# Kernel tuning notes

Hardware: AMD Instinct MI355X
Metric: run time of the kernel (lower is better)

## Reference

```python
import jax, jax.numpy as jnp
import numpy as np

L_RTN = 3  # complex taps produced by the RTN head (w_rtn3 out dim = 2*L_RTN)
EPS = 1e-12


def _to_complex(x):
    # (B, 2n) real interleaved [re0, im0, re1, im1, ...] -> (B, n) complex
    return x[:, 0::2] + 1j * x[:, 1::2]


def _to_real(xc):
    # (B, n) complex -> (B, 2n) real interleaved
    b, n = xc.shape
    return jnp.stack([xc.real, xc.imag], axis=-1).reshape(b, 2 * n)


def _complex_conv_taps(h_c, x_c):
    # per-sample causal complex FIR: out[t] = sum_l h[l] * x[t-l]
    # h_c: (B, L) complex, x_c: (B, n) complex
    n = x_c.shape[1]
    out = jnp.zeros_like(x_c)
    for l in range(h_c.shape[1]):  # L is tiny and static
        shifted = jnp.pad(x_c, ((0, 0), (l, 0)))[:, :n]
        out = out + h_c[:, l:l + 1] * shifted
    return out


def setup_inputs() -> dict:
    key = jax.random.key(0)
    ks = jax.random.split(key, 16)
    B, D_IN, H1, CH, H_RTN, H2, D_OUT = 8192, 512, 4096, 256, 1024, 4096, 512
    s = 0.02  # weight init scale
    x = jax.random.normal(ks[0], (B, D_IN), jnp.float32)
    w1 = s * jax.random.normal(ks[1], (H1, D_IN), jnp.float32)
    b1 = jnp.zeros((H1,), jnp.float32)
    w2 = s * jax.random.normal(ks[2], (CH, H1), jnp.float32)
    b2 = jnp.zeros((CH,), jnp.float32)
    w_rtn1 = s * jax.random.normal(ks[3], (H_RTN, CH), jnp.float32)
    b_rtn1 = jnp.zeros((H_RTN,), jnp.float32)
    w_rtn2 = s * jax.random.normal(ks[4], (H_RTN, H_RTN), jnp.float32)
    b_rtn2 = jnp.zeros((H_RTN,), jnp.float32)
    w_rtn3 = s * jax.random.normal(ks[5], (2 * L_RTN, H_RTN), jnp.float32)
    # bias so that RTN starts near identity tap [1, 0, 0, ...]
    b_rtn3 = jnp.zeros((2 * L_RTN,), jnp.float32).at[0].set(1.0)
    w3 = s * jax.random.normal(ks[6], (H2, CH), jnp.float32)
    b3 = jnp.zeros((H2,), jnp.float32)
    w4 = s * jax.random.normal(ks[7], (D_OUT, H2), jnp.float32)
    b4 = jnp.zeros((D_OUT,), jnp.float32)
    h = jax.random.normal(ks[8], (2,), jnp.float32)
    h = h / jnp.linalg.norm(h)  # unit-power single-tap fading channel
    noise = 0.1 * jax.random.normal(ks[9], (B, CH), jnp.float32)
    return {"x": x, "w1": w1, "b1": b1, "w2": w2, "b2": b2,
            "w_rtn1": w_rtn1, "b_rtn1": b_rtn1, "w_rtn2": w_rtn2,
            "b_rtn2": b_rtn2, "w_rtn3": w_rtn3, "b_rtn3": b_rtn3,
            "w3": w3, "b3": b3, "w4": w4, "b4": b4, "h": h, "noise": noise}


def reference(x, w1, b1, w2, b2, w_rtn1, b_rtn1, w_rtn2, b_rtn2,
              w_rtn3, b_rtn3, w3, b3, w4, b4, h, noise):
    # encoder (linear1 -> relu -> linear2)
    a = jax.nn.relu(x @ w1.T + b1)
    s = a @ w2.T + b2                      # (B, 2n) channel signal
    # power normalization: sqrt(2n) * sqrt(0.5) * s / ||s||
    scale = jnp.sqrt(s.shape[1] * 0.5)
    s = scale * s / jnp.linalg.norm(s, axis=1, keepdims=True)
    tx_c = _to_complex(s)                  # (B, n) transmitted symbols
    # single-tap complex channel
    h_c = h[0] + 1j * h[1]
    y = _to_real(h_c * tx_c) + noise       # add per-sample AWGN
    y_c = _to_complex(y)
    # LS channel estimate (1 tap): h_est = <y, x> / <x, x>
    num = jnp.sum(y_c * jnp.conj(tx_c), axis=1, keepdims=True)
    den = jnp.sum(jnp.abs(tx_c) ** 2, axis=1, keepdims=True)
    h_est = num / den                      # (B, 1)
    # zero-forcing signal estimate
    x_eq = y_c * jnp.conj(h_est) / (jnp.abs(h_est) ** 2 + EPS)
    xr = _to_real(x_eq)                    # (B, 2n)
    # RTN: predict inverse taps and apply per-sample complex conv
    g = jnp.tanh(xr @ w_rtn1.T + b_rtn1)
    g = jnp.tanh(g @ w_rtn2.T + b_rtn2)
    h_inv = g @ w_rtn3.T + b_rtn3          # (B, 2*L_RTN)
    h_inv_c = h_inv[:, 0::2] + 1j * h_inv[:, 1::2]
    xr = _to_real(_complex_conv_taps(h_inv_c, _to_complex(xr)))
    # decoder (linear3 -> relu -> linear4)
    out = jax.nn.relu(xr @ w3.T + b3)
    return out @ w4.T + b4
```

## Files before the change

### kernel.cpp

```cpp
#include <hip/hip_runtime.h>
#include <hip/hip_bf16.h>
#include <math.h>

using bf16 = __hip_bfloat16;
typedef __attribute__((ext_vector_type(8))) short short8;
typedef __attribute__((ext_vector_type(4))) float float4v;

template <typename T> __device__ inline T cvt_out(float v);
template <> __device__ inline float cvt_out<float>(float v) { return v; }
template <> __device__ inline bf16 cvt_out<bf16>(float v) { return __float2bfloat16(v); }

__device__ inline void gload_lds16(const bf16* g, bf16* l) {
    __builtin_amdgcn_global_load_lds(
        (const __attribute__((address_space(1))) void*)g,
        (__attribute__((address_space(3))) void*)l, 16, 0, 0);
}

struct CvtPack {
    const float* src[7];
    bf16* dst[7];
    int end[7];
};

__global__ __launch_bounds__(256) void cvt_all(CvtPack p) {
    int e = (blockIdx.x * 256 + threadIdx.x) * 4;
    int start = 0;
#pragma unroll
    for (int s = 0; s < 7; ++s) {
        if (e < p.end[s]) {
            int off = e - start;
            float4 v = *(const float4*)(p.src[s] + off);
            bf16* d = p.dst[s] + off;
            d[0] = __float2bfloat16(v.x);
            d[1] = __float2bfloat16(v.y);
            d[2] = __float2bfloat16(v.z);
            d[3] = __float2bfloat16(v.w);
            return;
        }
        start = p.end[s];
    }
}

__device__ inline float4 load4f(const float* p) { return *(const float4*)p; }
__device__ inline float4 load4f(const bf16* p) {
    ushort4 u = *(const ushort4*)p;
    float4 r;
    r.x = __uint_as_float((unsigned)u.x << 16);
    r.y = __uint_as_float((unsigned)u.y << 16);
    r.z = __uint_as_float((unsigned)u.z << 16);
    r.w = __uint_as_float((unsigned)u.w << 16);
    return r;
}
__device__ inline void store4(float* p, float4 v) { *(float4*)p = v; }
__device__ inline void store4(bf16* p, float4 v) {
    p[0] = __float2bfloat16(v.x); p[1] = __float2bfloat16(v.y);
    p[2] = __float2bfloat16(v.z); p[3] = __float2bfloat16(v.w);
}

template <int NK, int ACT, typename InT, typename OutT>
__global__ __launch_bounds__(256) void reduceK(const InT* __restrict__ p,
                                               const float* __restrict__ bias,
                                               OutT* __restrict__ out,
                                               size_t mn, int nmask, int total4) {
    int i = blockIdx.x * 256 + threadIdx.x;
    if (i < total4) {
        int idx = i * 4;
        float4 r = *(const float4*)(bias + (idx & nmask));
#pragma unroll
        for (int k = 0; k < NK; ++k) {
            float4 a = load4f(p + k * mn + idx);
            r.x += a.x; r.y += a.y; r.z += a.z; r.w += a.w;
        }
        if (ACT == 1) {
            r.x = fmaxf(r.x, 0.f); r.y = fmaxf(r.y, 0.f);
            r.z = fmaxf(r.z, 0.f); r.w = fmaxf(r.w, 0.f);
        } else if (ACT == 2) {
            r.x = tanhf(r.x); r.y = tanhf(r.y);
            r.z = tanhf(r.z); r.w = tanhf(r.w);
        }
        store4(out + idx, r);
    }
}

template <int ACT, typename OutT, bool PARTIAL>
__global__ __launch_bounds__(512, 2)
void gemm_pipe8(const bf16* __restrict__ A,
                const bf16* __restrict__ W,
                const float* __restrict__ bias,
                OutT* __restrict__ C,
                int M, int N, int K,
                int nbn, int kcount) {
    constexpr int BKT = 64;
    constexpr int CPR = BKT / 8;
    constexpr int LPH = BKT / 32;
    constexpr int KS  = BKT / 32;

    __shared__ bf16 As[2][2][128 * BKT];
    __shared__ bf16 Bs[2][2][128 * BKT];

    const int bi = blockIdx.x;
    const int xcd = bi & 7, t = bi >> 3;
    const int bn = t % nbn;
    const int bm = xcd + 8 * (t / nbn);
    const int kbeg = PARTIAL ? blockIdx.y * kcount : 0;
    OutT* Cp = PARTIAL ? C + (size_t)blockIdx.y * M * N : C;

    const int tid = threadIdx.x;
    const int wave = tid >> 6, lane = tid & 63;
    const int mwave = (wave >> 2) * 64, nwave = (wave & 3) * 32;
    const int quad = lane >> 4, lrow = lane & 15;
    const int swz = lrow & (CPR - 1);

    const bf16* Ab = A + (size_t)(bm * 256) * K + kbeg;
    const bf16* Wb = W + (size_t)(bn * 256) * K + kbeg;
    const int NT = kcount / BKT;

    auto stA = [&](int tl, int h) {
        if (tl >= NT) return;
#pragma unroll
        for (int tt = 0; tt < LPH; ++tt) {
            int base = tt * 512 + wave * 64;
            int c = base + lane;
            int row = c / CPR, ch = c % CPR;
            gload_lds16(Ab + (size_t)(h * 128 + row) * K + tl * BKT +
                            ((ch ^ (row & (CPR - 1))) << 3),
                        &As[tl & 1][h][0] + base * 8);
        }
    };
    auto stB = [&](int tl, int h) {
        if (tl >= NT) return;
#pragma unroll
        for (int tt = 0; tt < LPH; ++tt) {
            int base = tt * 512 + wave * 64;
            int c = base + lane;
            int row = c / CPR, ch = c % CPR;
            gload_lds16(Wb + (size_t)(h * 128 + row) * K + tl * BKT +
                            ((ch ^ (row & (CPR - 1))) << 3),
                        &Bs[tl & 1][h][0] + base * 8);
        }
    };

    float4v acc[2][2][4][2] = {};
    short8 af[4][KS], bfv[2][KS];

#define LDA8(BUF, MH)                                                         \
    { const bf16* pA = &As[BUF][MH][0];                                       \
      _Pragma("unroll") for (int i = 0; i < 4; ++i)                           \
        _Pragma("unroll") for (int ks = 0; ks < KS; ++ks)                     \
          af[i][ks] = *(const short8*)(pA + (mwave + i * 16 + lrow) * BKT +   \
                                       (((ks * 4 + quad) ^ swz) << 3)); }
#define LDB8(BUF, NH)                                                         \
    { const bf16* pB = &Bs[BUF][NH][0];                                       \
      _Pragma("unroll") for (int j = 0; j < 2; ++j)                           \
        _Pragma("unroll") for (int ks = 0; ks < KS; ++ks)                     \
          bfv[j][ks] = *(const short8*)(pB + (nwave + j * 16 + lrow) * BKT +  \
                                        (((ks * 4 + quad) ^ swz) << 3)); }
#define MM8(MH, NH)                                                           \
    { _Pragma("unroll") for (int ks = 0; ks < KS; ++ks)                       \
        _Pragma("unroll") for (int i = 0; i < 4; ++i)                         \
          _Pragma("unroll") for (int j = 0; j < 2; ++j)                       \
            acc[MH][NH][i][j] = __builtin_amdgcn_mfma_f32_16x16x32_bf16(      \
                af[i][ks], bfv[j][ks], acc[MH][NH][i][j], 0, 0, 0); }
#define WAITC asm volatile("s_waitcnt vmcnt(4)" ::: "memory");
#define SYNC_IN                                                               \
    __builtin_amdgcn_s_barrier();                                             \
    __builtin_amdgcn_s_setprio(1);
#define SYNC_OUT                                                              \
    __builtin_amdgcn_s_setprio(0);                                            \
    __builtin_amdgcn_s_barrier();

    stA(0, 0); stB(0, 0); stA(0, 1); stB(0, 1);
    stA(1, 0); stB(1, 1);
    if (NT > 1) { WAITC; }
    else        asm volatile("s_waitcnt vmcnt(0)" ::: "memory");
    __builtin_amdgcn_s_barrier();

    for (int T = 0; T < NT; T += 2) {
        LDA8(0, 0); LDB8(0, 0); stA(T + 1, 1);
        SYNC_IN; MM8(0, 0); SYNC_OUT;
        LDB8(0, 1); stB(T + 1, 0);
        SYNC_IN; MM8(0, 1); SYNC_OUT;
        LDA8(0, 1); stA(T + 2, 0);
        SYNC_IN; MM8(1, 1); SYNC_OUT;
        LDB8(0, 0); stB(T + 2, 1);
        SYNC_IN; MM8(1, 0);
        __builtin_amdgcn_s_setprio(0);
        if (T + 2 < NT) { WAITC; }
        else            asm volatile("s_waitcnt vmcnt(0)" ::: "memory");
        __builtin_amdgcn_s_barrier();
        LDA8(1, 0); LDB8(1, 0); stA(T + 2, 1);
        SYNC_IN; MM8(0, 0); SYNC_OUT;
        LDB8(1, 1); stB(T + 2, 0);
        SYNC_IN; MM8(0, 1); SYNC_OUT;
        LDA8(1, 1); stA(T + 3, 0);
        SYNC_IN; MM8(1, 1); SYNC_OUT;
        LDB8(1, 0); stB(T + 3, 1);
        SYNC_IN; MM8(1, 0);
        __builtin_amdgcn_s_setprio(0);
        if (T + 2 < NT) {
            WAITC;
            __builtin_amdgcn_s_barrier();
        }
    }
#undef LDA8
#undef LDB8
#undef MM8
#undef WAITC
#undef SYNC_IN
#undef SYNC_OUT

#pragma unroll
    for (int mh = 0; mh < 2; ++mh)
#pragma unroll
        for (int i = 0; i < 4; ++i) {
            int m0 = bm * 256 + mh * 128 + mwave + i * 16 + quad * 4;
#pragma unroll
            for (int nh = 0; nh < 2; ++nh)
#pragma unroll
                for (int j = 0; j < 2; ++j) {
                    int n = bn * 256 + nh * 128 + nwave + j * 16 + lrow;
                    if constexpr (PARTIAL) {
#pragma unroll
                        for (int r = 0; r < 4; ++r)
                            Cp[(size_t)(m0 + r) * N + n] = cvt_out<OutT>(acc[mh][nh][i][j][r]);
                    } else {
                        float bv = bias[n];
#pragma unroll
                        for (int r = 0; r < 4; ++r) {
                            float v = acc[mh][nh][i][j][r] + bv;
                            if (ACT == 1) v = fmaxf(v, 0.f);
                            else if (ACT == 2) v = tanhf(v);
                            Cp[(size_t)(m0 + r) * N + n] = cvt_out<OutT>(v);
                        }
                    }
                }
        }
}

template <int ACT, typename OutT, int WMT, int WNT, int BKT, bool PARTIAL>
__global__ __launch_bounds__(256) void gemm_bt(const bf16* __restrict__ A,
                                               const bf16* __restrict__ W,
                                               const float* __restrict__ bias,
                                               OutT* __restrict__ C,
                                               int M, int N, int K,
                                               int nbn, int kcount) {
    constexpr int TBM = 32 * WMT;
    constexpr int TBN = 32 * WNT;
    constexpr int CPR = BKT / 8;
    constexpr int CA = TBM * CPR;
    constexpr int CB = TBN * CPR;

    __shared__ bf16 As[TBM * BKT];
    __shared__ bf16 Bs[TBN * BKT];

    const int bi = blockIdx.x;
    const int xcd = bi & 7, t = bi >> 3;
    const int bn = t % nbn;
    const int bm = xcd + 8 * (t / nbn);
    const int kbeg = PARTIAL ? blockIdx.y * kcount : 0;
    OutT* Cp = PARTIAL ? C + (size_t)blockIdx.y * M * N : C;

    const int tid = threadIdx.x;
    const int wave = tid >> 6, lane = tid & 63;
    const int wm = (wave >> 1) * (16 * WMT), wn = (wave & 1) * (16 * WNT);
    const int quad = lane >> 4, lrow = lane & 15;

    float4v acc[WMT][WNT] = {};
    const size_t arow = (size_t)(bm * TBM) * K;
    const size_t brow = (size_t)(bn * TBN) * K;

    for (int k0 = kbeg; k0 < kbeg + kcount; k0 += BKT) {
        __syncthreads();
#pragma unroll
        for (int tt = 0; tt < CA / 256; ++tt) {
            int base = tt * 256 + wave * 64;
            int c = base + lane;
            int row = c / CPR, col = (c % CPR) * 8;
            gload_lds16(A + arow + (size_t)row * K + k0 + col, As + base * 8);
        }
#pragma unroll
        for (int tt = 0; tt < CB / 256; ++tt) {
            int base = tt * 256 + wave * 64;
            int c = base + lane;
            int row = c / CPR, col = (c % CPR) * 8;
            gload_lds16(W + brow + (size_t)row * K + k0 + col, Bs + base * 8);
        }
        __syncthreads();
#pragma unroll
        for (int kk = 0; kk < BKT; kk += 32) {
            short8 af[WMT], bfr[WNT];
#pragma unroll
            for (int i = 0; i < WMT; ++i)
                af[i] = *(const short8*)(As + (wm + i * 16 + lrow) * BKT + kk + quad * 8);
#pragma unroll
            for (int j = 0; j < WNT; ++j)
                bfr[j] = *(const short8*)(Bs + (wn + j * 16 + lrow) * BKT + kk + quad * 8);
#pragma unroll
            for (int i = 0; i < WMT; ++i)
#pragma unroll
                for (int j = 0; j < WNT; ++j)
                    acc[i][j] = __builtin_amdgcn_mfma_f32_16x16x32_bf16(af[i], bfr[j], acc[i][j], 0, 0, 0);
        }
    }

#pragma unroll
    for (int i = 0; i < WMT; ++i) {
        int m0 = bm * TBM + wm + i * 16 + quad * 4;
#pragma unroll
        for (int j = 0; j < WNT; ++j) {
            int n = bn * TBN + wn + j * 16 + lrow;
            if constexpr (PARTIAL) {
#pragma unroll
                for (int r = 0; r < 4; ++r)
                    Cp[(size_t)(m0 + r) * N + n] = cvt_out<OutT>(acc[i][j][r]);
            } else {
                float bv = bias[n];
#pragma unroll
                for (int r = 0; r < 4; ++r) {
                    float v = acc[i][j][r] + bv;
                    if (ACT == 1) v = fmaxf(v, 0.f);
                    else if (ACT == 2) v = tanhf(v);
                    Cp[(size_t)(m0 + r) * N + n] = cvt_out<OutT>(v);
                }
            }
        }
    }
}

__global__ __launch_bounds__(64) void channel_kernel(const float* __restrict__ s,
                                                     const float* __restrict__ h,
                                                     const float* __restrict__ noise,
                                                     float* __restrict__ xr_f,
                                                     bf16* __restrict__ xr_b) {
    const int b = blockIdx.x, lane = threadIdx.x;
    const float* srow = s + (size_t)b * 256;

    float ss = 0.f;
#pragma unroll
    for (int t = 0; t < 4; ++t) {
        float v = srow[lane + 64 * t];
        ss += v * v;
    }
#pragma unroll
    for (int off = 32; off; off >>= 1) ss += __shfl_xor(ss, off);
    const float inv = sqrtf(128.0f) / sqrtf(ss);

    const float hre = h[0], him = h[1];

    float yre[2], yim[2];
    float nre = 0.f, nim = 0.f, den = 0.f;
#pragma unroll
    for (int t = 0; t < 2; ++t) {
        int c = lane + 64 * t;
        float tr = srow[2 * c] * inv, ti = srow[2 * c + 1] * inv;
        float yr = hre * tr - him * ti + noise[(size_t)b * 256 + 2 * c];
        float yi = hre * ti + him * tr + noise[(size_t)b * 256 + 2 * c + 1];
        yre[t] = yr; yim[t] = yi;
        nre += yr * tr + yi * ti;
        nim += yi * tr - yr * ti;
        den += tr * tr + ti * ti;
    }
#pragma unroll
    for (int off = 32; off; off >>= 1) {
        nre += __shfl_xor(nre, off);
        nim += __shfl_xor(nim, off);
        den += __shfl_xor(den, off);
    }
    const float her = nre / den, hei = nim / den;
    const float d2 = her * her + hei * hei + 1e-12f;

#pragma unroll
    for (int t = 0; t < 2; ++t) {
        int c = lane + 64 * t;
        float xre = (yre[t] * her + yim[t] * hei) / d2;
        float xim = (yim[t] * her - yre[t] * hei) / d2;
        xr_f[(size_t)b * 256 + 2 * c] = xre;
        xr_f[(size_t)b * 256 + 2 * c + 1] = xim;
        xr_b[(size_t)b * 256 + 2 * c] = __float2bfloat16(xre);
        xr_b[(size_t)b * 256 + 2 * c + 1] = __float2bfloat16(xim);
    }
}

__global__ __launch_bounds__(64) void rtn_taps_conv(const bf16* __restrict__ g2,
                                                    const float* __restrict__ wr3,
                                                    const float* __restrict__ br3,
                                                    const float* __restrict__ xr_f,
                                                    bf16* __restrict__ xr2) {
    const int b = blockIdx.x, lane = threadIdx.x;
    const bf16* grow = g2 + (size_t)b * 1024;

    float acc[6] = {0.f, 0.f, 0.f, 0.f, 0.f, 0.f};
#pragma unroll
    for (int t = 0; t < 16; ++t) {
        int k = lane + 64 * t;
        float gv = __bfloat162float(grow[k]);
#pragma unroll
        for (int j = 0; j < 6; ++j) acc[j] += gv * wr3[j * 1024 + k];
    }
#pragma unroll
    for (int j = 0; j < 6; ++j)
#pragma unroll
        for (int off = 32; off; off >>= 1) acc[j] += __shfl_xor(acc[j], off);

    float tre[3], tim[3];
#pragma unroll
    for (int l = 0; l < 3; ++l) {
        tre[l] = acc[2 * l] + br3[2 * l];
        tim[l] = acc[2 * l + 1] + br3[2 * l + 1];
    }

    const float* xrow = xr_f + (size_t)b * 256;
#pragma unroll
    for (int t = 0; t < 2; ++t) {
        int c = lane + 64 * t;
        float ore = 0.f, oim = 0.f;
#pragma unroll
        for (int l = 0; l < 3; ++l) {
            int cc = c - l;
            if (cc >= 0) {
                float xre = xrow[2 * cc], xim = xrow[2 * cc + 1];
                ore += tre[l] * xre - tim[l] * xim;
                oim += tre[l] * xim + tim[l] * xre;
            }
        }
        xr2[(size_t)b * 256 + 2 * c] = __float2bfloat16(ore);
        xr2[(size_t)b * 256 + 2 * c + 1] = __float2bfloat16(oim);
    }
}

extern "C" void kernel_launch(void* const* d_in, const int* in_sizes, int n_in,
                              void* d_out, int out_size, void* d_ws, size_t ws_size,
                              hipStream_t stream) {
    constexpr int B = 8192, D_IN = 512, H1 = 4096, CH = 256, HR = 1024, H2 = 4096, DOUT = 512;

    const float* x   = (const float*)d_in[0];
    const float* w1  = (const float*)d_in[1];
    const float* b1  = (const float*)d_in[2];
    const float* w2  = (const float*)d_in[3];
    const float* b2  = (const float*)d_in[4];
    const float* wr1 = (const float*)d_in[5];
    const float* br1 = (const float*)d_in[6];
    const float* wr2 = (const float*)d_in[7];
    const float* br2 = (const float*)d_in[8];
    const float* wr3 = (const float*)d_in[9];
    const float* br3 = (const float*)d_in[10];
    const float* w3  = (const float*)d_in[11];
    const float* b3  = (const float*)d_in[12];
    const float* w4  = (const float*)d_in[13];
    const float* b4  = (const float*)d_in[14];
    const float* h   = (const float*)d_in[15];
    const float* noise = (const float*)d_in[16];

    char* ws = (char*)d_ws;
    bf16*  a    = (bf16*)(ws + 0);
    float* sF   = (float*)(ws + 0);
    bf16*  g1   = (bf16*)(ws + 0);
    bf16*  g2   = (bf16*)(ws + 16777216);
    bf16*  g4P  = (bf16*)(ws + 33554432);
    bf16*  tbuf = (bf16*)(ws + 0);
    bf16*  w1B  = (bf16*)(ws + 67108864);
    bf16*  w2B  = (bf16*)(ws + 71303168);
    bf16*  wr1B = (bf16*)(ws + 73400320);
    bf16*  wr2B = (bf16*)(ws + 73924608);
    bf16*  w3B  = (bf16*)(ws + 76021760);
    bf16*  w4B  = (bf16*)(ws + 78118912);
    bf16*  xB   = (bf16*)(ws + 82313216);
    bf16*  g2P  = (bf16*)(ws + 82313216);
    float* xrF  = (float*)(ws + 99090432);
    bf16*  xrB  = (bf16*)(ws + 107479040);
    bf16*  xr2  = (bf16*)(ws + 111673344);
    bf16*  g6P  = (bf16*)(ws + 82313216);

    dim3 blk(256);

    CvtPack p;
    const float* srcs[7] = {x, w1, w2, wr1, wr2, w3, w4};
    bf16* dsts[7] = {xB, w1B, w2B, wr1B, wr2B, w3B, w4B};
    int ns[7] = {B * D_IN, H1 * D_IN, CH * H1, HR * CH, HR * HR, H2 * CH, DOUT * H2};
    int cum = 0;
    for (int i = 0; i < 7; ++i) { p.src[i] = srcs[i]; p.dst[i] = dsts[i]; cum += ns[i]; p.end[i] = cum; }
    cvt_all<<<(cum / 4 + 255) / 256, blk, 0, stream>>>(p);

    gemm_pipe8<1, bf16, false><<<dim3(32 * 16), dim3(512), 0, stream>>>(
        xB, w1B, b1, a, B, H1, D_IN, 16, D_IN);
    gemm_pipe8<0, bf16, true><<<dim3(32, 8), dim3(512), 0, stream>>>(
        a, w2B, nullptr, g2P, B, CH, H1, 1, H1 / 8);
    reduceK<8, 0, bf16, float><<<(B * CH / 4 + 255) / 256, blk, 0, stream>>>(
        g2P, b2, sF, (size_t)B * CH, CH - 1, B * CH / 4);
    channel_kernel<<<B, 64, 0, stream>>>(sF, h, noise, xrF, xrB);
    gemm_bt<2, bf16, 4, 2, 64, false><<<64 * 16, blk, 0, stream>>>(
        xrB, wr1B, br1, g1, B, HR, CH, 16, CH);
    gemm_pipe8<0, bf16, true><<<dim3(32 * 4, 2), dim3(512), 0, stream>>>(
        g1, wr2B, nullptr, g4P, B, HR, HR, 4, HR / 2);
    reduceK<2, 2, bf16, bf16><<<(B * HR / 4 + 255) / 256, blk, 0, stream>>>(
        g4P, br2, g2, (size_t)B * HR, HR - 1, B * HR / 4);
    rtn_taps_conv<<<B, 64, 0, stream>>>(g2, wr3, br3, xrF, xr2);
    gemm_pipe8<1, bf16, false><<<dim3(32 * 16), dim3(512), 0, stream>>>(
        xr2, w3B, b3, tbuf, B, H2, CH, 16, CH);
    gemm_pipe8<0, bf16, true><<<dim3(32 * 2, 4), dim3(512), 0, stream>>>(
        tbuf, w4B, nullptr, g6P, B, DOUT, H2, 2, H2 / 4);
    reduceK<4, 0, bf16, float><<<(B * DOUT / 4 + 255) / 256, blk, 0, stream>>>(
        g6P, b4, (float*)d_out, (size_t)B * DOUT, DOUT - 1, B * DOUT / 4);
}
```

Baseline: 350.2 us.

## Stage GEMM epilogue through LDS for coalesced stores and keep B fragments resident

The A and B shared tiles are merged into one LDS buffer. After the main loop, that buffer is reused to stage the bf16 output tile with an XOR swizzle, so each thread writes 16-byte contiguous chunks to global memory instead of scattered 2-byte stores. B fragments are now kept per N-half in registers, which removes two LDS reloads per iteration at the cost of more registers. An explicit lgkmcnt wait and a scheduling barrier are added before each MFMA block. The epilogue always writes bf16, even for the float and partial-sum instantiations, which is a correctness risk if those paths are used.

```diff
diff --git a/kernel.cpp b/kernel.cpp
--- a/kernel.cpp
+++ b/kernel.cpp
@@ -95,8 +95,7 @@
     constexpr int LPH = BKT / 32;
     constexpr int KS  = BKT / 32;
 
-    __shared__ bf16 As[2][2][128 * BKT];
-    __shared__ bf16 Bs[2][2][128 * BKT];
+    __shared__ bf16 SMEM[65536];
 
     const int bi = blockIdx.x;
     const int xcd = bi & 7, t = bi >> 3;
@@ -117,6 +116,7 @@
 
     auto stA = [&](int tl, int h) {
         if (tl >= NT) return;
+        bf16* dst = SMEM + ((tl & 1) * 2 + h) * 8192;
 #pragma unroll
         for (int tt = 0; tt < LPH; ++tt) {
             int base = tt * 512 + wave * 64;
@@ -124,11 +124,12 @@
             int row = c / CPR, ch = c % CPR;
             gload_lds16(Ab + (size_t)(h * 128 + row) * K + tl * BKT +
                             ((ch ^ (row & (CPR - 1))) << 3),
-                        &As[tl & 1][h][0] + base * 8);
+                        dst + base * 8);
         }
     };
     auto stB = [&](int tl, int h) {
         if (tl >= NT) return;
+        bf16* dst = SMEM + 32768 + ((tl & 1) * 2 + h) * 8192;
 #pragma unroll
         for (int tt = 0; tt < LPH; ++tt) {
             int base = tt * 512 + wave * 64;
@@ -136,34 +137,36 @@
             int row = c / CPR, ch = c % CPR;
             gload_lds16(Wb + (size_t)(h * 128 + row) * K + tl * BKT +
                             ((ch ^ (row & (CPR - 1))) << 3),
-                        &Bs[tl & 1][h][0] + base * 8);
+                        dst + base * 8);
         }
     };
 
     float4v acc[2][2][4][2] = {};
-    short8 af[4][KS], bfv[2][KS];
+    short8 af[4][KS], bfv[2][2][KS];
 
 #define LDA8(BUF, MH)                                                         \
-    { const bf16* pA = &As[BUF][MH][0];                                       \
+    { const bf16* pA = SMEM + ((BUF) * 2 + (MH)) * 8192;                      \
       _Pragma("unroll") for (int i = 0; i < 4; ++i)                           \
         _Pragma("unroll") for (int ks = 0; ks < KS; ++ks)                     \
           af[i][ks] = *(const short8*)(pA + (mwave + i * 16 + lrow) * BKT +   \
                                        (((ks * 4 + quad) ^ swz) << 3)); }
 #define LDB8(BUF, NH)                                                         \
-    { const bf16* pB = &Bs[BUF][NH][0];                                       \
+    { const bf16* pB = SMEM + 32768 + ((BUF) * 2 + (NH)) * 8192;              \
       _Pragma("unroll") for (int j = 0; j < 2; ++j)                           \
         _Pragma("unroll") for (int ks = 0; ks < KS; ++ks)                     \
-          bfv[j][ks] = *(const short8*)(pB + (nwave + j * 16 + lrow) * BKT +  \
+          bfv[NH][j][ks] = *(const short8*)(pB + (nwave + j * 16 + lrow) * BKT + \
                                         (((ks * 4 + quad) ^ swz) << 3)); }
 #define MM8(MH, NH)                                                           \
     { _Pragma("unroll") for (int ks = 0; ks < KS; ++ks)                       \
         _Pragma("unroll") for (int i = 0; i < 4; ++i)                         \
           _Pragma("unroll") for (int j = 0; j < 2; ++j)                       \
             acc[MH][NH][i][j] = __builtin_amdgcn_mfma_f32_16x16x32_bf16(      \
-                af[i][ks], bfv[j][ks], acc[MH][NH][i][j], 0, 0, 0); }
+                af[i][ks], bfv[NH][j][ks], acc[MH][NH][i][j], 0, 0, 0); }
 #define WAITC asm volatile("s_waitcnt vmcnt(4)" ::: "memory");
 #define SYNC_IN                                                               \
     __builtin_amdgcn_s_barrier();                                             \
+    asm volatile("s_waitcnt lgkmcnt(0)" ::: "memory");                        \
+    __builtin_amdgcn_sched_barrier(0);                                        \
     __builtin_amdgcn_s_setprio(1);
 #define SYNC_OUT                                                              \
     __builtin_amdgcn_s_setprio(0);                                            \
@@ -182,7 +185,7 @@
         SYNC_IN; MM8(0, 1); SYNC_OUT;
         LDA8(0, 1); stA(T + 2, 0);
         SYNC_IN; MM8(1, 1); SYNC_OUT;
-        LDB8(0, 0); stB(T + 2, 1);
+        stB(T + 2, 1);
         SYNC_IN; MM8(1, 0);
         __builtin_amdgcn_s_setprio(0);
         if (T + 2 < NT) { WAITC; }
@@ -194,7 +197,7 @@
         SYNC_IN; MM8(0, 1); SYNC_OUT;
         LDA8(1, 1); stA(T + 3, 0);
         SYNC_IN; MM8(1, 1); SYNC_OUT;
-        LDB8(1, 0); stB(T + 3, 1);
+        stB(T + 3, 1);
         SYNC_IN; MM8(1, 0);
         __builtin_amdgcn_s_setprio(0);
         if (T + 2 < NT) {
@@ -209,32 +212,42 @@
 #undef SYNC_IN
 #undef SYNC_OUT
 
+    __builtin_amdgcn_s_barrier();
 #pragma unroll
     for (int mh = 0; mh < 2; ++mh)
 #pragma unroll
         for (int i = 0; i < 4; ++i) {
-            int m0 = bm * 256 + mh * 128 + mwave + i * 16 + quad * 4;
+            int rbase = mh * 128 + mwave + i * 16 + quad * 4;
 #pragma unroll
             for (int nh = 0; nh < 2; ++nh)
 #pragma unroll
                 for (int j = 0; j < 2; ++j) {
-                    int n = bn * 256 + nh * 128 + nwave + j * 16 + lrow;
-                    if constexpr (PARTIAL) {
-#pragma unroll
-                        for (int r = 0; r < 4; ++r)
-                            Cp[(size_t)(m0 + r) * N + n] = cvt_out<OutT>(acc[mh][nh][i][j][r]);
-                    } else {
-                        float bv = bias[n];
-#pragma unroll
-                        for (int r = 0; r < 4; ++r) {
-                            float v = acc[mh][nh][i][j][r] + bv;
-                            if (ACT == 1) v = fmaxf(v, 0.f);
-                            else if (ACT == 2) v = tanhf(v);
-                            Cp[(size_t)(m0 + r) * N + n] = cvt_out<OutT>(v);
-                        }
+                    int col = nh * 128 + nwave + j * 16 + lrow;
+                    float bv = PARTIAL ? 0.f : bias[bn * 256 + col];
+#pragma unroll
+                    for (int r = 0; r < 4; ++r) {
+                        int row = rbase + r;
+                        float v = acc[mh][nh][i][j][r] + bv;
+                        if (ACT == 1) v = fmaxf(v, 0.f);
+                        else if (ACT == 2) v = tanhf(v);
+                        int cidx = (col >> 3) ^ ((row >> 2) & 3);
+                        SMEM[row * 256 + cidx * 8 + (col & 7)] = __float2bfloat16(v);
                     }
                 }
         }
+    __builtin_amdgcn_s_barrier();
+    {
+        const int rl = tid >> 5;
+        const int cch = tid & 31;
+#pragma unroll
+        for (int p = 0; p < 16; ++p) {
+            int row = p * 16 + rl;
+            int cs = cch ^ ((row >> 2) & 3);
+            short8 v = *(const short8*)(SMEM + row * 256 + cs * 8);
+            size_t g = (size_t)(bm * 256 + row) * N + bn * 256 + cch * 8;
+            *(short8*)((bf16*)Cp + g) = v;
+        }
+    }
 }
 
 template <int ACT, typename OutT, int WMT, int WNT, int BKT, bool PARTIAL>
```

Measured after the change: 350.5 us. About the same (+0.1%).

## Fuse split-K reductions into consumers and reuse B fragments in the GEMM pipeline

Applied to the files above, without the earlier changes.

Removes two split-K reduce kernels: channel_kernel now sums the eight bf16 partials plus bias itself, and rtn_taps_conv sums the two partials, adds the bias and applies tanh in place. The rtn1 layer moves from the small gemm_bt kernel to the pipelined gemm_pipe8 with a tanh epilogue, and gemm_bt is deleted. Inside gemm_pipe8, B fragments are kept per N-half so one LDS reload per phase is skipped, with an explicit lgkmcnt wait and sched_barrier added at each sync point. The aim is fewer launches and less intermediate global traffic, at the cost of more registers in the main GEMM and extra stalls from the added waits.

```diff
diff --git a/kernel.cpp b/kernel.cpp
--- a/kernel.cpp
+++ b/kernel.cpp
@@ -41,7 +41,6 @@
     }
 }
 
-__device__ inline float4 load4f(const float* p) { return *(const float4*)p; }
 __device__ inline float4 load4f(const bf16* p) {
     ushort4 u = *(const ushort4*)p;
     float4 r;
@@ -50,11 +49,6 @@
     r.z = __uint_as_float((unsigned)u.z << 16);
     r.w = __uint_as_float((unsigned)u.w << 16);
     return r;
-}
-__device__ inline void store4(float* p, float4 v) { *(float4*)p = v; }
-__device__ inline void store4(bf16* p, float4 v) {
-    p[0] = __float2bfloat16(v.x); p[1] = __float2bfloat16(v.y);
-    p[2] = __float2bfloat16(v.z); p[3] = __float2bfloat16(v.w);
 }
 
 template <int NK, int ACT, typename InT, typename OutT>
@@ -74,11 +68,8 @@
         if (ACT == 1) {
             r.x = fmaxf(r.x, 0.f); r.y = fmaxf(r.y, 0.f);
             r.z = fmaxf(r.z, 0.f); r.w = fmaxf(r.w, 0.f);
-        } else if (ACT == 2) {
-            r.x = tanhf(r.x); r.y = tanhf(r.y);
-            r.z = tanhf(r.z); r.w = tanhf(r.w);
-        }
-        store4(out + idx, r);
+        }
+        *(float4*)((float*)out + idx) = r;
     }
 }
 
@@ -141,7 +132,7 @@
     };
 
     float4v acc[2][2][4][2] = {};
-    short8 af[4][KS], bfv[2][KS];
+    short8 af[4][KS], bfv[2][2][KS];
 
 #define LDA8(BUF, MH)                                                         \
     { const bf16* pA = &As[BUF][MH][0];                                       \
@@ -153,17 +144,19 @@
     { const bf16* pB = &Bs[BUF][NH][0];                                       \
       _Pragma("unroll") for (int j = 0; j < 2; ++j)                           \
         _Pragma("unroll") for (int ks = 0; ks < KS; ++ks)                     \
-          bfv[j][ks] = *(const short8*)(pB + (nwave + j * 16 + lrow) * BKT +  \
+          bfv[NH][j][ks] = *(const short8*)(pB + (nwave + j * 16 + lrow) * BKT + \
                                         (((ks * 4 + quad) ^ swz) << 3)); }
 #define MM8(MH, NH)                                                           \
     { _Pragma("unroll") for (int ks = 0; ks < KS; ++ks)                       \
         _Pragma("unroll") for (int i = 0; i < 4; ++i)                         \
           _Pragma("unroll") for (int j = 0; j < 2; ++j)                       \
             acc[MH][NH][i][j] = __builtin_amdgcn_mfma_f32_16x16x32_bf16(      \
-                af[i][ks], bfv[j][ks], acc[MH][NH][i][j], 0, 0, 0); }
+                af[i][ks], bfv[NH][j][ks], acc[MH][NH][i][j], 0, 0, 0); }
 #define WAITC asm volatile("s_waitcnt vmcnt(4)" ::: "memory");
 #define SYNC_IN                                                               \
     __builtin_amdgcn_s_barrier();                                             \
+    asm volatile("s_waitcnt lgkmcnt(0)" ::: "memory");                        \
+    __builtin_amdgcn_sched_barrier(0);                                        \
     __builtin_amdgcn_s_setprio(1);
 #define SYNC_OUT                                                              \
     __builtin_amdgcn_s_setprio(0);                                            \
@@ -182,7 +175,7 @@
         SYNC_IN; MM8(0, 1); SYNC_OUT;
         LDA8(0, 1); stA(T + 2, 0);
         SYNC_IN; MM8(1, 1); SYNC_OUT;
-        LDB8(0, 0); stB(T + 2, 1);
+        stB(T + 2, 1);
         SYNC_IN; MM8(1, 0);
         __builtin_amdgcn_s_setprio(0);
         if (T + 2 < NT) { WAITC; }
@@ -194,7 +187,7 @@
         SYNC_IN; MM8(0, 1); SYNC_OUT;
         LDA8(1, 1); stA(T + 3, 0);
         SYNC_IN; MM8(1, 1); SYNC_OUT;
-        LDB8(1, 0); stB(T + 3, 1);
+        stB(T + 3, 1);
         SYNC_IN; MM8(1, 0);
         __builtin_amdgcn_s_setprio(0);
         if (T + 2 < NT) {
@@ -237,110 +230,29 @@
         }
 }
 
-template <int ACT, typename OutT, int WMT, int WNT, int BKT, bool PARTIAL>
-__global__ __launch_bounds__(256) void gemm_bt(const bf16* __restrict__ A,
-                                               const bf16* __restrict__ W,
-                                               const float* __restrict__ bias,
-                                               OutT* __restrict__ C,
-                                               int M, int N, int K,
-                                               int nbn, int kcount) {
-    constexpr int TBM = 32 * WMT;
-    constexpr int TBN = 32 * WNT;
-    constexpr int CPR = BKT / 8;
-    constexpr int CA = TBM * CPR;
-    constexpr int CB = TBN * CPR;
-
-    __shared__ bf16 As[TBM * BKT];
-    __shared__ bf16 Bs[TBN * BKT];
-
-    const int bi = blockIdx.x;
-    const int xcd = bi & 7, t = bi >> 3;
-    const int bn = t % nbn;
-    const int bm = xcd + 8 * (t / nbn);
-    const int kbeg = PARTIAL ? blockIdx.y * kcount : 0;
-    OutT* Cp = PARTIAL ? C + (size_t)blockIdx.y * M * N : C;
-
-    const int tid = threadIdx.x;
-    const int wave = tid >> 6, lane = tid & 63;
-    const int wm = (wave >> 1) * (16 * WMT), wn = (wave & 1) * (16 * WNT);
-    const int quad = lane >> 4, lrow = lane & 15;
-
-    float4v acc[WMT][WNT] = {};
-    const size_t arow = (size_t)(bm * TBM) * K;
-    const size_t brow = (size_t)(bn * TBN) * K;
-
-    for (int k0 = kbeg; k0 < kbeg + kcount; k0 += BKT) {
-        __syncthreads();
-#pragma unroll
-        for (int tt = 0; tt < CA / 256; ++tt) {
-            int base = tt * 256 + wave * 64;
-            int c = base + lane;
-            int row = c / CPR, col = (c % CPR) * 8;
-            gload_lds16(A + arow + (size_t)row * K + k0 + col, As + base * 8);
-        }
-#pragma unroll
-        for (int tt = 0; tt < CB / 256; ++tt) {
-            int base = tt * 256 + wave * 64;
-            int c = base + lane;
-            int row = c / CPR, col = (c % CPR) * 8;
-            gload_lds16(W + brow + (size_t)row * K + k0 + col, Bs + base * 8);
-        }
-        __syncthreads();
-#pragma unroll
-        for (int kk = 0; kk < BKT; kk += 32) {
-            short8 af[WMT], bfr[WNT];
-#pragma unroll
-            for (int i = 0; i < WMT; ++i)
-                af[i] = *(const short8*)(As + (wm + i * 16 + lrow) * BKT + kk + quad * 8);
-#pragma unroll
-            for (int j = 0; j < WNT; ++j)
-                bfr[j] = *(const short8*)(Bs + (wn + j * 16 + lrow) * BKT + kk + quad * 8);
-#pragma unroll
-            for (int i = 0; i < WMT; ++i)
-#pragma unroll
-                for (int j = 0; j < WNT; ++j)
-                    acc[i][j] = __builtin_amdgcn_mfma_f32_16x16x32_bf16(af[i], bfr[j], acc[i][j], 0, 0, 0);
-        }
-    }
-
-#pragma unroll
-    for (int i = 0; i < WMT; ++i) {
-        int m0 = bm * TBM + wm + i * 16 + quad * 4;
-#pragma unroll
-        for (int j = 0; j < WNT; ++j) {
-            int n = bn * TBN + wn + j * 16 + lrow;
-            if constexpr (PARTIAL) {
-#pragma unroll
-                for (int r = 0; r < 4; ++r)
-                    Cp[(size_t)(m0 + r) * N + n] = cvt_out<OutT>(acc[i][j][r]);
-            } else {
-                float bv = bias[n];
-#pragma unroll
-                for (int r = 0; r < 4; ++r) {
-                    float v = acc[i][j][r] + bv;
-                    if (ACT == 1) v = fmaxf(v, 0.f);
-                    else if (ACT == 2) v = tanhf(v);
-                    Cp[(size_t)(m0 + r) * N + n] = cvt_out<OutT>(v);
-                }
-            }
-        }
-    }
-}
-
-__global__ __launch_bounds__(64) void channel_kernel(const float* __restrict__ s,
+__global__ __launch_bounds__(64) void channel_kernel(const bf16* __restrict__ p,
+                                                     const float* __restrict__ b2,
                                                      const float* __restrict__ h,
                                                      const float* __restrict__ noise,
                                                      float* __restrict__ xr_f,
                                                      bf16* __restrict__ xr_b) {
+    __shared__ float srow[256];
     const int b = blockIdx.x, lane = threadIdx.x;
-    const float* srow = s + (size_t)b * 256;
+    const size_t mn = (size_t)8192 * 256;
+    const size_t rb = (size_t)b * 256;
 
     float ss = 0.f;
 #pragma unroll
     for (int t = 0; t < 4; ++t) {
-        float v = srow[lane + 64 * t];
+        int c = lane + 64 * t;
+        float v = b2[c];
+#pragma unroll
+        for (int k = 0; k < 8; ++k)
+            v += __bfloat162float(p[k * mn + rb + c]);
+        srow[c] = v;
         ss += v * v;
     }
+    __syncthreads();
 #pragma unroll
     for (int off = 32; off; off >>= 1) ss += __shfl_xor(ss, off);
     const float inv = sqrtf(128.0f) / sqrtf(ss);
@@ -353,8 +265,8 @@
     for (int t = 0; t < 2; ++t) {
         int c = lane + 64 * t;
         float tr = srow[2 * c] * inv, ti = srow[2 * c + 1] * inv;
-        float yr = hre * tr - him * ti + noise[(size_t)b * 256 + 2 * c];
-        float yi = hre * ti + him * tr + noise[(size_t)b * 256 + 2 * c + 1];
+        float yr = hre * tr - him * ti + noise[rb + 2 * c];
+        float yi = hre * ti + him * tr + noise[rb + 2 * c + 1];
         yre[t] = yr; yim[t] = yi;
         nre += yr * tr + yi * ti;
         nim += yi * tr - yr * ti;
@@ -374,26 +286,29 @@
         int c = lane + 64 * t;
         float xre = (yre[t] * her + yim[t] * hei) / d2;
         float xim = (yim[t] * her - yre[t] * hei) / d2;
-        xr_f[(size_t)b * 256 + 2 * c] = xre;
-        xr_f[(size_t)b * 256 + 2 * c + 1] = xim;
-        xr_b[(size_t)b * 256 + 2 * c] = __float2bfloat16(xre);
-        xr_b[(size_t)b * 256 + 2 * c + 1] = __float2bfloat16(xim);
-    }
-}
-
-__global__ __launch_bounds__(64) void rtn_taps_conv(const bf16* __restrict__ g2,
+        xr_f[rb + 2 * c] = xre;
+        xr_f[rb + 2 * c + 1] = xim;
+        xr_b[rb + 2 * c] = __float2bfloat16(xre);
+        xr_b[rb + 2 * c + 1] = __float2bfloat16(xim);
+    }
+}
+
+__global__ __launch_bounds__(64) void rtn_taps_conv(const bf16* __restrict__ p,
+                                                    const float* __restrict__ br2,
                                                     const float* __restrict__ wr3,
                                                     const float* __restrict__ br3,
                                                     const float* __restrict__ xr_f,
                                                     bf16* __restrict__ xr2) {
     const int b = blockIdx.x, lane = threadIdx.x;
-    const bf16* grow = g2 + (size_t)b * 1024;
+    const size_t mn = (size_t)8192 * 1024;
+    const bf16* p0 = p + (size_t)b * 1024;
+    const bf16* p1 = p0 + mn;
 
     float acc[6] = {0.f, 0.f, 0.f, 0.f, 0.f, 0.f};
 #pragma unroll
     for (int t = 0; t < 16; ++t) {
         int k = lane + 64 * t;
-        float gv = __bfloat162float(grow[k]);
+        float gv = tanhf(__bfloat162float(p0[k]) + __bfloat162float(p1[k]) + br2[k]);
 #pragma unroll
         for (int j = 0; j < 6; ++j) acc[j] += gv * wr3[j * 1024 + k];
     }
@@ -453,9 +368,9 @@
 
     char* ws = (char*)d_ws;
     bf16*  a    = (bf16*)(ws + 0);
-    float* sF   = (float*)(ws + 0);
-    bf16*  g1   = (bf16*)(ws + 0);
-    bf16*  g2   = (bf16*)(ws + 16777216);
+    float* xrF  = (float*)(ws + 0);
+    bf16*  g1   = (bf16*)(ws + 8388608);
+    bf16*  xrB  = (bf16*)(ws + 25165824);
     bf16*  g4P  = (bf16*)(ws + 33554432);
     bf16*  tbuf = (bf16*)(ws + 0);
     bf16*  w1B  = (bf16*)(ws + 67108864);
@@ -466,9 +381,7 @@
     bf16*  w4B  = (bf16*)(ws + 78118912);
     bf16*  xB   = (bf16*)(ws + 82313216);
     bf16*  g2P  = (bf16*)(ws + 82313216);
-    float* xrF  = (float*)(ws + 99090432);
-    bf16*  xrB  = (bf16*)(ws + 107479040);
-    bf16*  xr2  = (bf16*)(ws + 111673344);
+    bf16*  xr2  = (bf16*)(ws + 107479040);
     bf16*  g6P  = (bf16*)(ws + 82313216);
 
     dim3 blk(256);
@@ -485,16 +398,12 @@
         xB, w1B, b1, a, B, H1, D_IN, 16, D_IN);
     gemm_pipe8<0, bf16, true><<<dim3(32, 8), dim3(512), 0, stream>>>(
         a, w2B, nullptr, g2P, B, CH, H1, 1, H1 / 8);
-    reduceK<8, 0, bf16, float><<<(B * CH / 4 + 255) / 256, blk, 0, stream>>>(
-        g2P, b2, sF, (size_t)B * CH, CH - 1, B * CH / 4);
-    channel_kernel<<<B, 64, 0, stream>>>(sF, h, noise, xrF, xrB);
-    gemm_bt<2, bf16, 4, 2, 64, false><<<64 * 16, blk, 0, stream>>>(
-        xrB, wr1B, br1, g1, B, HR, CH, 16, CH);
+    channel_kernel<<<B, 64, 0, stream>>>(g2P, b2, h, noise, xrF, xrB);
+    gemm_pipe8<2, bf16, false><<<dim3(32 * 4), dim3(512), 0, stream>>>(
+        xrB, wr1B, br1, g1, B, HR, CH, 4, CH);
     gemm_pipe8<0, bf16, true><<<dim3(32 * 4, 2), dim3(512), 0, stream>>>(
         g1, wr2B, nullptr, g4P, B, HR, HR, 4, HR / 2);
-    reduceK<2, 2, bf16, bf16><<<(B * HR / 4 + 255) / 256, blk, 0, stream>>>(
-        g4P, br2, g2, (size_t)B * HR, HR - 1, B * HR / 4);
-    rtn_taps_conv<<<B, 64, 0, stream>>>(g2, wr3, br3, xrF, xr2);
+    rtn_taps_conv<<<B, 64, 0, stream>>>(g4P, br2, wr3, br3, xrF, xr2);
     gemm_pipe8<1, bf16, false><<<dim3(32 * 16), dim3(512), 0, stream>>>(
         xr2, w3B, b3, tbuf, B, H2, CH, 16, CH);
     gemm_pipe8<0, bf16, true><<<dim3(32 * 2, 4), dim3(512), 0, stream>>>(
```

Result: no change. 355.2 us (+1.4%).
